# Performance work log

Measured on AMD Instinct MI355X. Metric: run time of the kernel, lower is better.

## Reference

```python
import jax, jax.numpy as jnp
import numpy as np

B, N, D = 32, 1024, 256
NHID = 512
NHID_HALF = NHID // 2
NCLASS = 2


def _xavier(key, shape):
    fan_in, fan_out = shape
    lim = float(np.sqrt(6.0 / (fan_in + fan_out)))
    return jax.random.uniform(key, shape, jnp.float32, -lim, lim)


def setup_inputs() -> dict:
    key = jax.random.key(0)
    ks = jax.random.split(key, 10)
    x = jax.random.normal(ks[0], (B, N, D), jnp.float32)
    adj = jax.random.uniform(ks[1], (B, N, N), jnp.float32)
    adj = adj / jnp.sum(adj, axis=-1, keepdims=True)  # row-normalized (mean aggregation)
    # GraphConv weights: shape (2*in_dim, out_dim) due to concat([x, agg(x)])
    W1 = _xavier(ks[2], (2 * D, NHID))
    b1 = jnp.zeros((NHID,), jnp.float32)
    W2 = _xavier(ks[3], (2 * NHID, NHID))
    b2 = jnp.zeros((NHID,), jnp.float32)
    W3 = _xavier(ks[4], (2 * NHID, NHID_HALF))
    b3 = jnp.zeros((NHID_HALF,), jnp.float32)
    W4 = _xavier(ks[5], (2 * NHID_HALF, NHID_HALF))
    b4 = jnp.zeros((NHID_HALF,), jnp.float32)
    # classifier: Linear(256,256) + PReLU(256) + Linear(256,2)
    cW1 = _xavier(ks[6], (NHID_HALF, NHID_HALF))
    cb1 = jnp.zeros((NHID_HALF,), jnp.float32)
    alpha = jnp.full((NHID_HALF,), 0.25, jnp.float32)
    cW2 = _xavier(ks[7], (NHID_HALF, NCLASS))
    cb2 = jnp.zeros((NCLASS,), jnp.float32)
    return {"x": x, "adj": adj, "W1": W1, "b1": b1, "W2": W2, "b2": b2,
            "W3": W3, "b3": b3, "W4": W4, "b4": b4,
            "cW1": cW1, "cb1": cb1, "alpha": alpha, "cW2": cW2, "cb2": cb2}


def _graphconv(x, adj, W, b):
    agg = jnp.einsum('bnm,bmd->bnd', adj, x)          # mean aggregation (adj row-normalized)
    cat = jnp.concatenate([x, agg], axis=-1)          # [B, N, 2*d]
    return jax.nn.relu(jnp.einsum('bnd,df->bnf', cat, W) + b)


def reference(x, adj, W1, b1, W2, b2, W3, b3, W4, b4, cW1, cb1, alpha, cW2, cb2):
    h = _graphconv(x, adj, W1, b1)
    h = _graphconv(h, adj, W2, b2)
    h = _graphconv(h, adj, W3, b3)
    h = _graphconv(h, adj, W4, b4)
    # classifier MLP with channel-wise PReLU
    h = jnp.einsum('bnd,df->bnf', h, cW1) + cb1
    h = jnp.where(h > 0, h, alpha * h)
    pred = jnp.einsum('bnd,df->bnf', h, cW2) + cb2
    return pred
```

## Files before the change

kernel.cpp:

```cpp
#include <hip/hip_runtime.h>

typedef short v8s __attribute__((ext_vector_type(8)));
typedef _Float16 v8h __attribute__((ext_vector_type(8)));
typedef float v4f __attribute__((ext_vector_type(4)));

#define BMT 128
#define BNT 128
#define BKT 32

__device__ __forceinline__ unsigned short f2bf(float f) {
    unsigned int u = __float_as_uint(f);
    u += 0x7fff + ((u >> 16) & 1);
    return (unsigned short)(u >> 16);
}
__device__ __forceinline__ unsigned short f2h(float f) {
    union { _Float16 h; unsigned short u; } c;
    c.h = (_Float16)f;
    return c.u;
}
__device__ __forceinline__ float h2f(unsigned short v) {
    union { unsigned short u; _Float16 h; } c;
    c.u = v;
    return (float)c.h;
}
__device__ __forceinline__ v8h as_h(v8s x) {
    union { v8s s; v8h h; } c;
    c.s = x;
    return c.h;
}

union U128 { unsigned short s[8]; uint4 v; };

__device__ __forceinline__ void gld16(const unsigned short* g, unsigned short* l) {
    __builtin_amdgcn_global_load_lds((const __attribute__((address_space(1))) void*)g,
                                     (__attribute__((address_space(3))) void*)l, 16, 0, 0);
}

__global__ __launch_bounds__(256) void split_f16(const float* __restrict__ x,
                                                 unsigned short* __restrict__ o, int n4) {
    int i = blockIdx.x * 256 + threadIdx.x;
    if (i < n4) {
        float4 f = ((const float4*)x)[i];
        float fv[4] = {f.x, f.y, f.z, f.w};
        ushort4 h;
        unsigned short* hp = (unsigned short*)&h;
#pragma unroll
        for (int j = 0; j < 4; ++j) hp[j] = f2h(fv[j]);
        ((ushort4*)o)[i] = h;
    }
}

__global__ __launch_bounds__(256) void split_hi(const float* __restrict__ x,
                                                unsigned short* __restrict__ oh, int n4) {
    int i = blockIdx.x * 256 + threadIdx.x;
    if (i < n4) {
        float4 f = ((const float4*)x)[i];
        float fv[4] = {f.x, f.y, f.z, f.w};
        ushort4 h;
        unsigned short* hp = (unsigned short*)&h;
#pragma unroll
        for (int j = 0; j < 4; ++j) hp[j] = f2bf(fv[j]);
        ((ushort4*)oh)[i] = h;
    }
}

__global__ __launch_bounds__(256) void tsplit16(const float* __restrict__ W,
                                                unsigned short* __restrict__ th, int R, int C) {
    int e = blockIdx.x * 256 + threadIdx.x;
    if (e < R * C) {
        int k = e / C, n = e - k * C;
        th[(size_t)n * R + k] = f2h(W[e]);
    }
}

__global__ __launch_bounds__(256) void transp_x(const float* __restrict__ src,
                                                unsigned short* __restrict__ th, int d) {
    __shared__ unsigned int lds[64 * 66];
    const int t = threadIdx.x;
    const int mt = blockIdx.x, ft = blockIdx.y, z = blockIdx.z;
    const int r = t >> 3, c8 = (t & 7) * 8;
#pragma unroll
    for (int half = 0; half < 2; ++half) {
        int rr = r + half * 32;
        size_t grow = (size_t)z * 1024 + mt * 64 + rr;
        const float* xs = src + grow * d + ft * 64 + c8;
        float4 f0 = *(const float4*)xs;
        float4 f1 = *(const float4*)(xs + 4);
        float fv[8] = {f0.x, f0.y, f0.z, f0.w, f1.x, f1.y, f1.z, f1.w};
#pragma unroll
        for (int j = 0; j < 8; ++j)
            lds[rr * 66 + c8 + j] = f2bf(fv[j]);
    }
    __syncthreads();
    const int f = t >> 3, m0 = (t & 7) * 8;
#pragma unroll
    for (int half = 0; half < 2; ++half) {
        int ff = f + half * 32;
        U128 uh;
#pragma unroll
        for (int j = 0; j < 8; ++j)
            uh.s[j] = (unsigned short)lds[(m0 + j) * 66 + ff];
        size_t orow = ((size_t)z * d + ft * 64 + ff) * 1024 + mt * 64 + m0;
        *(uint4*)(th + orow) = uh.v;
    }
}

template <int ACT, bool TWO, int AMODE, int DT, bool WRT>
__global__ __launch_bounds__(256) void gemm128(
    const void* a1, const unsigned short* __restrict__ a2,
    int K1, int K2,
    const unsigned short* __restrict__ b_, int ldb,
    const float* __restrict__ bias, const float* __restrict__ alpha,
    unsigned short* __restrict__ o_, int Nout,
    unsigned short* __restrict__ th,
    size_t aZ, size_t bZ, int cZRows,
    int nblk, int mBits)
{
    constexpr int LA = (AMODE == 0) ? 32 : 40;
    constexpr int LB = 32;
    __shared__ __align__(16) unsigned short Ash[BMT * LA];
    __shared__ __align__(16) unsigned short Bsh[BNT * LB];

    const int t = threadIdx.x;
    const int lane = t & 63, wave = t >> 6;
    const int wm = wave >> 1, wn = wave & 1;
    const int l15 = lane & 15, quad = lane >> 4;

    const int bx = blockIdx.x;
    const int low3 = bx & 7, rest = bx >> 3;
    const int nIdx = rest % nblk, g = rest / nblk;
    const int grp = g * 8 + low3;
    const int m0 = (grp & ((1 << mBits) - 1)) * BMT;
    const int zb = grp >> mBits;
    const int n0 = nIdx * BNT;

    const unsigned short* bhz = b_ + (size_t)zb * bZ;

    v4f acc[4][4] = {};

    const int nch = TWO ? 2 : 1;
    for (int ch = 0; ch < nch; ++ch) {
        const int K = (TWO && ch) ? K2 : K1;
        const int kr0 = (TWO && ch) ? K1 : 0;
        const unsigned short* ah = nullptr;
        const float* af = nullptr;
        if constexpr (AMODE == 0)
            ah = (ch ? a2 : (const unsigned short*)a1) + (size_t)zb * aZ;
        else
            af = (const float*)a1 + (size_t)zb * aZ;

        for (int kk = 0; kk < K; kk += BKT) {
            __syncthreads();
            if constexpr (AMODE == 0) {
#pragma unroll
                for (int i = 0; i < 2; ++i) {
                    int s = i * 256 + t;
                    int row = s >> 2;
                    int cg = (s & 3) ^ ((s >> 3) & 3);
                    size_t go = (size_t)(m0 + row) * K + kk + cg * 8;
                    int ls = (i * 256 + (t & ~63)) * 8;
                    gld16(ah + go, &Ash[ls]);
                }
            } else {
#pragma unroll
                for (int i = 0; i < 2; ++i) {
                    int cid = i * 256 + t;
                    int row = cid >> 2, c = cid & 3;
                    const float* src = af + (size_t)(m0 + row) * K + kk + c * 8;
                    float4 f0 = *(const float4*)src;
                    float4 f1 = *(const float4*)(src + 4);
                    float fv[8] = {f0.x, f0.y, f0.z, f0.w, f1.x, f1.y, f1.z, f1.w};
                    U128 uh;
#pragma unroll
                    for (int j = 0; j < 8; ++j) uh.s[j] = f2bf(fv[j]);
                    *(uint4*)&Ash[row * LA + c * 8] = uh.v;
                }
            }
#pragma unroll
            for (int i = 0; i < 2; ++i) {
                int s = i * 256 + t;
                int row = s >> 2;
                int cg = (s & 3) ^ ((s >> 3) & 3);
                size_t go = (size_t)(n0 + row) * ldb + kr0 + kk + cg * 8;
                int ls = (i * 256 + (t & ~63)) * 8;
                gld16(bhz + go, &Bsh[ls]);
            }
            __syncthreads();
            v8s ahf[4];
#pragma unroll
            for (int mi = 0; mi < 4; ++mi) {
                int row = wm * 64 + mi * 16 + l15;
                int off;
                if constexpr (AMODE == 0) off = row * LA + ((quad ^ ((row >> 1) & 3)) * 8);
                else                      off = row * LA + quad * 8;
                ahf[mi] = *(const v8s*)&Ash[off];
            }
#pragma unroll
            for (int ni = 0; ni < 4; ++ni) {
                int row = wn * 64 + ni * 16 + l15;
                int off = row * LB + ((quad ^ ((row >> 1) & 3)) * 8);
                v8s bhf = *(const v8s*)&Bsh[off];
#pragma unroll
                for (int mi = 0; mi < 4; ++mi) {
                    if constexpr (DT == 0)
                        acc[mi][ni] = __builtin_amdgcn_mfma_f32_16x16x32_bf16(ahf[mi], bhf, acc[mi][ni], 0, 0, 0);
                    else
                        acc[mi][ni] = __builtin_amdgcn_mfma_f32_16x16x32_f16(as_h(ahf[mi]), as_h(bhf), acc[mi][ni], 0, 0, 0);
                }
            }
        }
    }

    const size_t crow0 = (size_t)zb * cZRows + m0;
#pragma unroll
    for (int ni = 0; ni < 4; ++ni) {
        int n = n0 + wn * 64 + ni * 16 + l15;
        float bv = (ACT > 0) ? bias[n] : 0.f;
        float av = (ACT == 2) ? alpha[n] : 0.f;
#pragma unroll
        for (int mi = 0; mi < 4; ++mi) {
#pragma unroll
            for (int r = 0; r < 4; ++r) {
                int m = wm * 64 + mi * 16 + quad * 4 + r;
                float v = acc[mi][ni][r] + bv;
                if (ACT == 1) v = v > 0.f ? v : 0.f;
                if (ACT == 2) v = v > 0.f ? v : av * v;
                acc[mi][ni][r] = v;
                o_[(crow0 + m) * (size_t)Nout + n] = f2h(v);
            }
        }
    }

    if constexpr (WRT) {
        const int zbT = m0 >> 10;
        const int mloc0 = (m0 & 1023) + wm * 64;
#pragma unroll
        for (int ni = 0; ni < 4; ++ni) {
            int f = n0 + wn * 64 + ni * 16 + l15;
            size_t rowb = (((size_t)zbT * Nout + f) << 10) + mloc0;
#pragma unroll
            for (int mi = 0; mi < 4; ++mi) {
                ushort4 u;
                unsigned short* up = (unsigned short*)&u;
#pragma unroll
                for (int r = 0; r < 4; ++r) up[r] = f2bf(acc[mi][ni][r]);
                *(ushort4*)(th + rowb + mi * 16 + quad * 4) = u;
            }
        }
    }
}

__global__ __launch_bounds__(256) void final_gemm(const unsigned short* __restrict__ hh,
                                                  const float* __restrict__ W,
                                                  const float* __restrict__ bias,
                                                  float* __restrict__ out) {
    const int t = threadIdx.x;
    const int m = blockIdx.x * 64 + (t >> 2);
    const int kq = (t & 3) * 64;
    const unsigned short* ph = hh + (size_t)m * 256 + kq;
    float a0 = 0.f, a1 = 0.f;
#pragma unroll
    for (int i = 0; i < 8; ++i) {
        uint4 vh = *(const uint4*)(ph + i * 8);
        const unsigned short* sh = (const unsigned short*)&vh;
#pragma unroll
        for (int j = 0; j < 8; ++j) {
            int k = kq + i * 8 + j;
            float h = h2f(sh[j]);
            a0 += h * W[k * 2];
            a1 += h * W[k * 2 + 1];
        }
    }
    a0 += __shfl_down(a0, 2); a0 += __shfl_down(a0, 1);
    a1 += __shfl_down(a1, 2); a1 += __shfl_down(a1, 1);
    if ((t & 3) == 0) {
        out[(size_t)m * 2] = a0 + bias[0];
        out[(size_t)m * 2 + 1] = a1 + bias[1];
    }
}

extern "C" void kernel_launch(void* const* d_in, const int* in_sizes, int n_in,
                              void* d_out, int out_size, void* d_ws, size_t ws_size,
                              hipStream_t stream) {
    const float* x   = (const float*)d_in[0];
    const float* adj = (const float*)d_in[1];
    const float* W1  = (const float*)d_in[2];
    const float* b1  = (const float*)d_in[3];
    const float* W2  = (const float*)d_in[4];
    const float* b2  = (const float*)d_in[5];
    const float* W3  = (const float*)d_in[6];
    const float* b3  = (const float*)d_in[7];
    const float* W4  = (const float*)d_in[8];
    const float* b4  = (const float*)d_in[9];
    const float* cW1 = (const float*)d_in[10];
    const float* cb1 = (const float*)d_in[11];
    const float* alp = (const float*)d_in[12];
    const float* cW2 = (const float*)d_in[13];
    const float* cb2 = (const float*)d_in[14];
    float* out = (float*)d_out;

    const size_t P   = 32768ull * 512;
    const size_t XP  = 32768ull * 256;
    const size_t WT_TOT = 1245184;
    const size_t ADJ = 32ull * 1024 * 1024;

    unsigned short* N1  = (unsigned short*)d_ws;
    unsigned short* N2  = N1 + P;
    unsigned short* N3  = N2 + P;
    unsigned short* Th  = N3 + P;
    unsigned short* X16 = Th + P;
    unsigned short* WT  = X16 + XP;
    unsigned short* SA  = WT + WT_TOT;

    const size_t o1 = 0, o2 = 262144, o3 = 786432, o4 = 1048576, o5 = 1179648;
    const bool preAdj = ws_size >= (4 * P + XP + WT_TOT + ADJ) * sizeof(unsigned short);

    dim3 blk(256);

    split_f16<<<8192, blk, 0, stream>>>(x, X16, (int)(XP / 4));
    tsplit16<<<1024, blk, 0, stream>>>(W1,  WT + o1, 512, 512);
    tsplit16<<<2048, blk, 0, stream>>>(W2,  WT + o2, 1024, 512);
    tsplit16<<<1024, blk, 0, stream>>>(W3,  WT + o3, 1024, 256);
    tsplit16<<<512,  blk, 0, stream>>>(W4,  WT + o4, 512, 256);
    tsplit16<<<256,  blk, 0, stream>>>(cW1, WT + o5, 256, 256);
    if (preAdj)
        split_hi<<<32768, blk, 0, stream>>>(adj, SA, (int)(ADJ / 4));

    transp_x<<<dim3(16, 4, 32), blk, 0, stream>>>(x, Th, 256);
    if (preAdj)
        gemm128<0, false, 0, 0, false><<<512, blk, 0, stream>>>(
            SA, nullptr, 1024, 0, Th, 1024, nullptr, nullptr,
            N2, 256, nullptr, (size_t)1 << 20, 256ull * 1024, 1024, 2, 3);
    else
        gemm128<0, false, 1, 0, false><<<512, blk, 0, stream>>>(
            adj, nullptr, 1024, 0, Th, 1024, nullptr, nullptr,
            N2, 256, nullptr, (size_t)1 << 20, 256ull * 1024, 1024, 2, 3);
    gemm128<1, true, 0, 1, true><<<1024, blk, 0, stream>>>(
        X16, N2, 256, 256, WT + o1, 512, b1, nullptr,
        N3, 512, Th, 0, 0, 0, 4, 8);
    if (preAdj)
        gemm128<0, false, 0, 0, false><<<1024, blk, 0, stream>>>(
            SA, nullptr, 1024, 0, Th, 1024, nullptr, nullptr,
            N1, 512, nullptr, (size_t)1 << 20, 512ull * 1024, 1024, 4, 3);
    else
        gemm128<0, false, 1, 0, false><<<1024, blk, 0, stream>>>(
            adj, nullptr, 1024, 0, Th, 1024, nullptr, nullptr,
            N1, 512, nullptr, (size_t)1 << 20, 512ull * 1024, 1024, 4, 3);
    gemm128<1, true, 0, 1, true><<<1024, blk, 0, stream>>>(
        N3, N1, 512, 512, WT + o2, 1024, b2, nullptr,
        N2, 512, Th, 0, 0, 0, 4, 8);
    if (preAdj)
        gemm128<0, false, 0, 0, false><<<1024, blk, 0, stream>>>(
            SA, nullptr, 1024, 0, Th, 1024, nullptr, nullptr,
            N1, 512, nullptr, (size_t)1 << 20, 512ull * 1024, 1024, 4, 3);
    else
        gemm128<0, false, 1, 0, false><<<1024, blk, 0, stream>>>(
            adj, nullptr, 1024, 0, Th, 1024, nullptr, nullptr,
            N1, 512, nullptr, (size_t)1 << 20, 512ull * 1024, 1024, 4, 3);
    gemm128<1, true, 0, 1, true><<<512, blk, 0, stream>>>(
        N2, N1, 512, 512, WT + o3, 1024, b3, nullptr,
        N3, 256, Th, 0, 0, 0, 2, 8);
    if (preAdj)
        gemm128<0, false, 0, 0, false><<<512, blk, 0, stream>>>(
            SA, nullptr, 1024, 0, Th, 1024, nullptr, nullptr,
            N1, 256, nullptr, (size_t)1 << 20, 256ull * 1024, 1024, 2, 3);
    else
        gemm128<0, false, 1, 0, false><<<512, blk, 0, stream>>>(
            adj, nullptr, 1024, 0, Th, 1024, nullptr, nullptr,
            N1, 256, nullptr, (size_t)1 << 20, 256ull * 1024, 1024, 2, 3);
    gemm128<1, true, 0, 1, false><<<512, blk, 0, stream>>>(
        N3, N1, 256, 256, WT + o4, 512, b4, nullptr,
        N2, 256, nullptr, 0, 0, 0, 2, 8);
    gemm128<2, false, 0, 1, false><<<512, blk, 0, stream>>>(
        N2, nullptr, 256, 0, WT + o5, 256, cb1, alp,
        N3, 256, nullptr, 0, 0, 0, 2, 8);
    final_gemm<<<512, blk, 0, stream>>>(N3, cW2, cb2, out);
}
```

Baseline: 642.4 us.

## Add 256-row, 512-thread GEMM kernel with 4-stage pipeline for all layers

Introduces a gemm256 kernel that uses 512-thread blocks, 256xBN2 output tiles (BN2 = 128 or 256) and a four-slot LDS ring with three tiles prefetched ahead. The waits use explicit vmcnt values. All aggregation and feature GEMMs on the preAdj path move to this kernel, with grids of 256 blocks. The larger tiles are meant to raise operand reuse and cut global traffic, and the deeper pipeline aims to hide load latency. In exchange the kernel needs more LDS and registers, and launching only 256 blocks may leave CUs underused.

```diff
diff --git a/kernel.cpp b/kernel.cpp
--- a/kernel.cpp
+++ b/kernel.cpp
@@ -240,6 +240,162 @@
             size_t rowb = (((size_t)zbT * Nout + f) << 10) + mloc0;
 #pragma unroll
             for (int mi = 0; mi < 4; ++mi) {
+                ushort4 u;
+                unsigned short* up = (unsigned short*)&u;
+#pragma unroll
+                for (int r = 0; r < 4; ++r) up[r] = f2bf(acc[mi][ni][r]);
+                *(ushort4*)(th + rowb + mi * 16 + quad * 4) = u;
+            }
+        }
+    }
+}
+
+template <int ACT, bool TWO, int DT, bool WRT, int BN2>
+__global__ __launch_bounds__(512, 2) void gemm256(
+    const unsigned short* __restrict__ a1, const unsigned short* __restrict__ a2,
+    int K1, int K2,
+    const unsigned short* __restrict__ b_, int ldb,
+    const float* __restrict__ bias, const float* __restrict__ alpha,
+    unsigned short* __restrict__ o_, int Nout,
+    unsigned short* __restrict__ th,
+    size_t aZ, size_t bZ, int cZRows,
+    int nblk, int mBits)
+{
+    constexpr int ASLOT = 256 * 32;
+    constexpr int BSLOT = BN2 * 32;
+    constexpr int SLOT  = ASLOT + BSLOT;
+    constexpr int LPT   = 2 + BN2 / 128;
+    constexpr int WN    = BN2 / 64;
+    constexpr int WM    = 8 / WN;
+    constexpr int MREP  = 16 / WM;
+    __shared__ __align__(16) unsigned short lds[4 * SLOT];
+
+    const int t = threadIdx.x;
+    const int lane = t & 63, wave = t >> 6;
+    const int wm = wave / WN, wn = wave % WN;
+    const int l15 = lane & 15, quad = lane >> 4;
+
+    const int bx = blockIdx.x;
+    const int low3 = bx & 7, rest = bx >> 3;
+    const int nIdx = rest % nblk, g = rest / nblk;
+    const int grp = g * 8 + low3;
+    const int m0 = (grp & ((1 << mBits) - 1)) * 256;
+    const int zb = grp >> mBits;
+    const int n0 = nIdx * BN2;
+
+    const unsigned short* A1 = a1 + (size_t)zb * aZ;
+    const unsigned short* A2p = TWO ? (a2 + (size_t)zb * aZ) : nullptr;
+    const unsigned short* B = b_ + (size_t)zb * bZ;
+
+    const int NT1 = K1 >> 5;
+    const int NTtot = NT1 + (TWO ? (K2 >> 5) : 0);
+
+    auto stage = [&](int tt) {
+        unsigned short* slot = &lds[(tt & 3) * SLOT];
+        const unsigned short* abase;
+        int astr;
+        if constexpr (TWO) {
+            if (tt >= NT1) { abase = A2p + ((size_t)(tt - NT1) << 5); astr = K2; }
+            else           { abase = A1 + ((size_t)tt << 5); astr = K1; }
+        } else {
+            abase = A1 + ((size_t)tt << 5); astr = K1;
+        }
+#pragma unroll
+        for (int i = 0; i < 2; ++i) {
+            int s = i * 512 + t;
+            int row = s >> 2;
+            int cg = (s & 3) ^ ((s >> 3) & 3);
+            gld16(abase + (size_t)(m0 + row) * astr + cg * 8,
+                  &slot[(i * 512 + (t & ~63)) * 8]);
+        }
+        const unsigned short* bbase = B + ((size_t)tt << 5);
+#pragma unroll
+        for (int i = 0; i < BN2 / 128; ++i) {
+            int s = i * 512 + t;
+            int row = s >> 2;
+            int cg = (s & 3) ^ ((s >> 3) & 3);
+            gld16(bbase + (size_t)(n0 + row) * ldb + cg * 8,
+                  &slot[ASLOT + (i * 512 + (t & ~63)) * 8]);
+        }
+    };
+
+    v4f acc[MREP][4] = {};
+
+    const int npro = NTtot < 3 ? NTtot : 3;
+    for (int tt = 0; tt < npro; ++tt) stage(tt);
+
+    for (int tt = 0; tt < NTtot; ++tt) {
+        const int rem = NTtot - 1 - tt;
+        if (rem >= 2) {
+            if constexpr (LPT == 4) asm volatile("s_waitcnt vmcnt(8)" ::: "memory");
+            else                    asm volatile("s_waitcnt vmcnt(6)" ::: "memory");
+        } else if (rem == 1) {
+            if constexpr (LPT == 4) asm volatile("s_waitcnt vmcnt(4)" ::: "memory");
+            else                    asm volatile("s_waitcnt vmcnt(3)" ::: "memory");
+        } else {
+            asm volatile("s_waitcnt vmcnt(0)" ::: "memory");
+        }
+        __builtin_amdgcn_s_barrier();
+        asm volatile("" ::: "memory");
+
+        if (tt + 3 < NTtot) stage(tt + 3);
+
+        const unsigned short* slot = &lds[(tt & 3) * SLOT];
+        v8s af[MREP];
+#pragma unroll
+        for (int mi = 0; mi < MREP; ++mi) {
+            int row = wm * (MREP * 16) + mi * 16 + l15;
+            af[mi] = *(const v8s*)&slot[row * 32 + ((quad ^ ((row >> 1) & 3)) * 8)];
+        }
+        v8s bf[4];
+#pragma unroll
+        for (int ni = 0; ni < 4; ++ni) {
+            int row = wn * 64 + ni * 16 + l15;
+            bf[ni] = *(const v8s*)&slot[ASLOT + row * 32 + ((quad ^ ((row >> 1) & 3)) * 8)];
+        }
+        __builtin_amdgcn_s_setprio(1);
+#pragma unroll
+        for (int ni = 0; ni < 4; ++ni) {
+#pragma unroll
+            for (int mi = 0; mi < MREP; ++mi) {
+                if constexpr (DT == 0)
+                    acc[mi][ni] = __builtin_amdgcn_mfma_f32_16x16x32_bf16(af[mi], bf[ni], acc[mi][ni], 0, 0, 0);
+                else
+                    acc[mi][ni] = __builtin_amdgcn_mfma_f32_16x16x32_f16(as_h(af[mi]), as_h(bf[ni]), acc[mi][ni], 0, 0, 0);
+            }
+        }
+        __builtin_amdgcn_s_setprio(0);
+    }
+
+    const size_t crow0 = (size_t)zb * cZRows + m0;
+#pragma unroll
+    for (int ni = 0; ni < 4; ++ni) {
+        int n = n0 + wn * 64 + ni * 16 + l15;
+        float bv = (ACT > 0) ? bias[n] : 0.f;
+        float av = (ACT == 2) ? alpha[n] : 0.f;
+#pragma unroll
+        for (int mi = 0; mi < MREP; ++mi) {
+#pragma unroll
+            for (int r = 0; r < 4; ++r) {
+                int m = wm * (MREP * 16) + mi * 16 + quad * 4 + r;
+                float v = acc[mi][ni][r] + bv;
+                if (ACT == 1) v = v > 0.f ? v : 0.f;
+                if (ACT == 2) v = v > 0.f ? v : av * v;
+                acc[mi][ni][r] = v;
+                o_[(crow0 + m) * (size_t)Nout + n] = f2h(v);
+            }
+        }
+    }
+
+    if constexpr (WRT) {
+        const int zbT = m0 >> 10;
+        const int mloc0 = (m0 & 1023) + wm * (MREP * 16);
+#pragma unroll
+        for (int ni = 0; ni < 4; ++ni) {
+            int f = n0 + wn * 64 + ni * 16 + l15;
+            size_t rowb = (((size_t)zbT * Nout + f) << 10) + mloc0;
+#pragma unroll
+            for (int mi = 0; mi < MREP; ++mi) {
                 ushort4 u;
                 unsigned short* up = (unsigned short*)&u;
 #pragma unroll
@@ -316,6 +472,7 @@
     const bool preAdj = ws_size >= (4 * P + XP + WT_TOT + ADJ) * sizeof(unsigned short);
 
     dim3 blk(256);
+    dim3 blk5(512);
 
     split_f16<<<8192, blk, 0, stream>>>(x, X16, (int)(XP / 4));
     tsplit16<<<1024, blk, 0, stream>>>(W1,  WT + o1, 512, 512);
@@ -327,52 +484,62 @@
         split_hi<<<32768, blk, 0, stream>>>(adj, SA, (int)(ADJ / 4));
 
     transp_x<<<dim3(16, 4, 32), blk, 0, stream>>>(x, Th, 256);
+
     if (preAdj)
-        gemm128<0, false, 0, 0, false><<<512, blk, 0, stream>>>(
+        gemm256<0, false, 0, false, 128><<<256, blk5, 0, stream>>>(
             SA, nullptr, 1024, 0, Th, 1024, nullptr, nullptr,
-            N2, 256, nullptr, (size_t)1 << 20, 256ull * 1024, 1024, 2, 3);
+            N2, 256, nullptr, (size_t)1 << 20, 256ull * 1024, 1024, 2, 2);
     else
         gemm128<0, false, 1, 0, false><<<512, blk, 0, stream>>>(
             adj, nullptr, 1024, 0, Th, 1024, nullptr, nullptr,
             N2, 256, nullptr, (size_t)1 << 20, 256ull * 1024, 1024, 2, 3);
-    gemm128<1, true, 0, 1, true><<<1024, blk, 0, stream>>>(
+
+    gemm256<1, true, 1, true, 256><<<256, blk5, 0, stream>>>(
         X16, N2, 256, 256, WT + o1, 512, b1, nullptr,
-        N3, 512, Th, 0, 0, 0, 4, 8);
+        N3, 512, Th, 0, 0, 0, 2, 7);
+
     if (preAdj)
-        gemm128<0, false, 0, 0, false><<<1024, blk, 0, stream>>>(
+        gemm256<0, false, 0, false, 256><<<256, blk5, 0, stream>>>(
             SA, nullptr, 1024, 0, Th, 1024, nullptr, nullptr,
-            N1, 512, nullptr, (size_t)1 << 20, 512ull * 1024, 1024, 4, 3);
+            N1, 512, nullptr, (size_t)1 << 20, 512ull * 1024, 1024, 2, 2);
     else
         gemm128<0, false, 1, 0, false><<<1024, blk, 0, stream>>>(
             adj, nullptr, 1024, 0, Th, 1024, nullptr, nullptr,
             N1, 512, nullptr, (size_t)1 << 20, 512ull * 1024, 1024, 4, 3);
-    gemm128<1, true, 0, 1, true><<<1024, blk, 0, stream>>>(
+
+    gemm256<1, true, 1, true, 256><<<256, blk5, 0, stream>>>(
         N3, N1, 512, 512, WT + o2, 1024, b2, nullptr,
-        N2, 512, Th, 0, 0, 0, 4, 8);
+        N2, 512, Th, 0, 0, 0, 2, 7);
+
     if (preAdj)
-        gemm128<0, false, 0, 0, false><<<1024, blk, 0, stream>>>(
+        gemm256<0, false, 0, false, 256><<<256, blk5, 0, stream>>>(
             SA, nullptr, 1024, 0, Th, 1024, nullptr, nullptr,
-            N1, 512, nullptr, (size_t)1 << 20, 512ull * 1024, 1024, 4, 3);
+            N1, 512, nullptr, (size_t)1 << 20, 512ull * 1024, 1024, 2, 2);
     else
         gemm128<0, false, 1, 0, false><<<1024, blk, 0, stream>>>(
             adj, nullptr, 1024, 0, Th, 1024, nullptr, nullptr,
             N1, 512, nullptr, (size_t)1 << 20, 512ull * 1024, 1024, 4, 3);
-    gemm128<1, true, 0, 1, true><<<512, blk, 0, stream>>>(
+
+    gemm256<1, true, 1, true, 128><<<256, blk5, 0, stream>>>(
         N2, N1, 512, 512, WT + o3, 1024, b3, nullptr,
-        N3, 256, Th, 0, 0, 0, 2, 8);
+        N3, 256, Th, 0, 0, 0, 2, 7);
+
     if (preAdj)
-        gemm128<0, false, 0, 0, false><<<512, blk, 0, stream>>>(
+        gemm256<0, false, 0, false, 128><<<256, blk5, 0, stream>>>(
             SA, nullptr, 1024, 0, Th, 1024, nullptr, nullptr,
-            N1, 256, nullptr, (size_t)1 << 20, 256ull * 1024, 1024, 2, 3);
+            N1, 256, nullptr, (size_t)1 << 20, 256ull * 1024, 1024, 2, 2);
     else
         gemm128<0, false, 1, 0, false><<<512, blk, 0, stream>>>(
             adj, nullptr, 1024, 0, Th, 1024, nullptr, nullptr,
             N1, 256, nullptr, (size_t)1 << 20, 256ull * 1024, 1024, 2, 3);
-    gemm128<1, true, 0, 1, false><<<512, blk, 0, stream>>>(
+
+    gemm256<1, true, 1, false, 128><<<256, blk5, 0, stream>>>(
         N3, N1, 256, 256, WT + o4, 512, b4, nullptr,
-        N2, 256, nullptr, 0, 0, 0, 2, 8);
-    gemm128<2, false, 0, 1, false><<<512, blk, 0, stream>>>(
+        N2, 256, nullptr, 0, 0, 0, 2, 7);
+
+    gemm256<2, false, 1, false, 128><<<256, blk5, 0, stream>>>(
         N2, nullptr, 256, 0, WT + o5, 256, cb1, alp,
-        N3, 256, nullptr, 0, 0, 0, 2, 8);
+        N3, 256, nullptr, 0, 0, 0, 2, 7);
+
     final_gemm<<<512, blk, 0, stream>>>(N3, cW2, cb2, out);
 }
```

Measured after the change: 559.0 us. -13.0%, faster.
